# Kernel tuning notes

Hardware: AMD Instinct MI355X
Metric: run time of the kernel (lower is better)

Reference implementation:

```python
import jax, jax.numpy as jnp
import numpy as np

WS = 7           # window size
NH = 12          # num heads
EPS_ADA = 1e-6   # AdaLayerNorm eps
EPS_LN = 1e-5    # torch nn.LayerNorm default eps


def _rel_pos_index(ws):
    coords = np.stack(np.meshgrid(np.arange(ws), np.arange(ws), indexing='ij'))  # (2,ws,ws)
    flat = coords.reshape(2, -1)                      # (2, N)
    rel = flat[:, :, None] - flat[:, None, :]         # (2, N, N)
    rel = rel.transpose(1, 2, 0).astype(np.int64)     # (N, N, 2)
    rel[:, :, 0] += ws - 1
    rel[:, :, 1] += ws - 1
    rel[:, :, 0] *= 2 * ws - 1
    return jnp.asarray(rel.sum(-1))                   # (N, N) in [0, (2ws-1)^2)

REL_IDX = _rel_pos_index(WS)


def setup_inputs() -> dict:
    key = jax.random.key(0)
    ks = jax.random.split(key, 8)
    B, H, W, C, COND = 32, 56, 56, 384, 128
    L = H * W
    s = 0.02
    return {
        'x_tok': jax.random.normal(ks[0], (B, L, C), jnp.float32),
        'z_tok': jax.random.normal(ks[1], (B, L, C), jnp.float32),
        'cond': jax.random.normal(ks[2], (B, COND), jnp.float32),
        'gamma_x': jnp.ones((C,), jnp.float32),
        'beta_x': jnp.zeros((C,), jnp.float32),
        'mod_w': jax.random.normal(ks[3], (COND, 2 * C), jnp.float32) * s,
        'mod_b': jnp.zeros((2 * C,), jnp.float32),
        'gamma_z': jnp.ones((C,), jnp.float32),
        'beta_z': jnp.zeros((C,), jnp.float32),
        'rel_bias_table': jax.random.normal(ks[4], ((2 * WS - 1) ** 2, NH), jnp.float32) * s,
        'q_w': jax.random.normal(ks[5], (C, C), jnp.float32) * s,
        'q_b': jnp.zeros((C,), jnp.float32),
        'kv_w': jax.random.normal(ks[6], (C, 2 * C), jnp.float32) * s,
        'kv_b': jnp.zeros((2 * C,), jnp.float32),
        'proj_w': jax.random.normal(ks[7], (C, C), jnp.float32) * s,
        'proj_b': jnp.zeros((C,), jnp.float32),
        'H': H,
        'W': W,
    }


def reference(x_tok, z_tok, cond, gamma_x, beta_x, mod_w, mod_b,
              gamma_z, beta_z, rel_bias_table, q_w, q_b, kv_w, kv_b,
              proj_w, proj_b, H, W):
    B, L, C = x_tok.shape
    hd = C // NH
    N = WS * WS

    # AdaLayerNorm-Zero on x
    mu = x_tok.mean(-1, keepdims=True)
    var = ((x_tok - mu) ** 2).mean(-1, keepdims=True)
    x_hat = (x_tok - mu) * jax.lax.rsqrt(var + EPS_ADA)
    mod = (cond @ mod_w + mod_b).reshape(B, 2, C)
    d_gamma, d_beta = mod[:, 0], mod[:, 1]
    x = (gamma_x * (1.0 + d_gamma))[:, None, :] * x_hat + (beta_x + d_beta)[:, None, :]

    # LayerNorm on z
    mz = z_tok.mean(-1, keepdims=True)
    vz = ((z_tok - mz) ** 2).mean(-1, keepdims=True)
    z = (z_tok - mz) * jax.lax.rsqrt(vz + EPS_LN) * gamma_z + beta_z

    # window partition: (B,H,W,C) -> (B*nW, N, C)
    def part(t):
        t = t.reshape(B, H // WS, WS, W // WS, WS, C)
        return t.transpose(0, 1, 3, 2, 4, 5).reshape(-1, N, C)

    x_win = part(x.reshape(B, H, W, C))
    z_win = part(z.reshape(B, H, W, C))

    # cross window attention
    q = (x_win @ q_w + q_b).reshape(-1, N, NH, hd).transpose(0, 2, 1, 3)  # (Bw,H,N,d)
    kv = (z_win @ kv_w + kv_b).reshape(-1, N, 2, NH, hd)
    k = kv[:, :, 0].transpose(0, 2, 1, 3)
    v = kv[:, :, 1].transpose(0, 2, 1, 3)
    scale = hd ** -0.5
    attn = jnp.einsum('bhnd,bhmd->bhnm', q * scale, k)                    # (Bw,H,N,N)
    bias = rel_bias_table[REL_IDX.reshape(-1)].reshape(N, N, NH).transpose(2, 0, 1)
    attn = jax.nn.softmax(attn + bias[None], axis=-1)
    out = jnp.einsum('bhnm,bhmd->bhnd', attn, v).transpose(0, 2, 1, 3).reshape(-1, N, C)
    out = out @ proj_w + proj_b

    # window reverse: (B*nW, N, C) -> (B, L, C)
    fused = out.reshape(B, H // WS, W // WS, WS, WS, C)
    fused = fused.transpose(0, 1, 3, 2, 4, 5).reshape(B, L, C)

    return x_tok + fused
```

## Files before the change

### kernel.cpp

```cpp
#include <hip/hip_runtime.h>
#include <hip/hip_bf16.h>

typedef float f32x4 __attribute__((ext_vector_type(4)));
typedef short short8 __attribute__((ext_vector_type(8)));
typedef __hip_bfloat16 bf16;

constexpr int CDIM  = 384;
constexpr int LTOK  = 3136;
constexpr int NWIN  = 2048;
constexpr int MROWS = 100352;
constexpr int MPAD  = MROWS + 64;

__device__ __forceinline__ void gload_lds16(const void* g, void* l) {
  __builtin_amdgcn_global_load_lds(
      (const __attribute__((address_space(1))) void*)g,
      (__attribute__((address_space(3))) void*)l, 16, 0, 0);
}

__device__ __forceinline__ void row_to_bl(int r, int& b, int& l) {
  int w = r / 49, n = r % 49;
  b = w >> 6;
  int wrem = w & 63;
  int wy = wrem >> 3, wx = wrem & 7;
  int ny = n / 7, nx = n % 7;
  l = (wy * 7 + ny) * 56 + wx * 7 + nx;
}


__global__ __launch_bounds__(256) void mod_kernel(
    const float* __restrict__ cond, const float* __restrict__ mw,
    const float* __restrict__ mb, float* __restrict__ mod) {
  int idx = blockIdx.x * 256 + threadIdx.x;
  int b = idx / 768, j = idx % 768;
  float s = mb[j];
  const float* cr = cond + b * 128;
  #pragma unroll 4
  for (int k = 0; k < 128; k++) s += cr[k] * mw[(size_t)k * 768 + j];
  mod[idx] = s;
}

__global__ __launch_bounds__(256) void prep_wt(
    const float* __restrict__ qw, const float* __restrict__ kvw,
    const float* __restrict__ pw,
    bf16* __restrict__ wtq, bf16* __restrict__ wtkv, bf16* __restrict__ wtp) {
  int idx = blockIdx.x * 256 + threadIdx.x;
  const float* src; bf16* dst; int i, Wn;
  if (idx < 147456)      { i = idx;          src = qw;  dst = wtq;  Wn = 384; }
  else if (idx < 442368) { i = idx - 147456; src = kvw; dst = wtkv; Wn = 768; }
  else                   { i = idx - 442368; src = pw;  dst = wtp;  Wn = 384; }
  int chunk = i / 12288, rem = i % 12288;
  int kt = rem >> 10, rem2 = rem & 1023;
  int ni = (rem2 >> 9) & 1, g = (rem2 >> 7) & 3, r16 = (rem2 >> 3) & 15, j = rem2 & 7;
  int k = kt * 32 + g * 8 + j, n = chunk * 32 + ni * 16 + r16;
  dst[i] = __float2bfloat16(src[(size_t)k * Wn + n]);
}

__global__ __launch_bounds__(256) void bias_kernel(
    const float* __restrict__ tab, float* __restrict__ bT) {
  int idx = blockIdx.x * 256 + threadIdx.x;
  int h = idx >> 12, rem = idx & 4095, m = rem >> 6, c = rem & 63;
  float v;
  if (c >= 49)      v = -1e30f;
  else if (m >= 49) v = 0.f;
  else {
    int yq = m / 7, xq = m % 7, yk = c / 7, xk = c % 7;
    v = tab[((yq - yk + 6) * 13 + (xq - xk + 6)) * 12 + h];
  }
  bT[idx] = v;
}


struct alignas(8) B4 { bf16 h[4]; };

__global__ __launch_bounds__(256) void ln_kernel(
    const float* __restrict__ src, const float* __restrict__ gamma,
    const float* __restrict__ beta, const float* __restrict__ mod,
    float eps, bf16* __restrict__ dst) {
  int wid = threadIdx.x >> 6, lane = threadIdx.x & 63;
  int r = blockIdx.x * 4 + wid;
  int bb, ll; row_to_bl(r, bb, ll);
  const f32x4* x4 = (const f32x4*)(src + ((size_t)bb * LTOK + ll) * 384);
  f32x4 a = x4[lane];
  f32x4 b = {0.f, 0.f, 0.f, 0.f};
  if (lane < 32) b = x4[64 + lane];
  float s  = a[0] + a[1] + a[2] + a[3] + b[0] + b[1] + b[2] + b[3];
  float s2 = a[0]*a[0] + a[1]*a[1] + a[2]*a[2] + a[3]*a[3]
           + b[0]*b[0] + b[1]*b[1] + b[2]*b[2] + b[3]*b[3];
  #pragma unroll
  for (int d = 1; d < 64; d <<= 1) { s += __shfl_xor(s, d); s2 += __shfl_xor(s2, d); }
  float mu = s * (1.f / 384.f);
  float var = s2 * (1.f / 384.f) - mu * mu;
  float rstd = rsqrtf(var + eps);
  bf16* o = dst + (size_t)r * 384;
  const f32x4* g4 = (const f32x4*)gamma;
  const f32x4* be4 = (const f32x4*)beta;
  if (mod != nullptr) {
    const f32x4* mg4 = (const f32x4*)(mod + bb * 768);
    const f32x4* mb4 = (const f32x4*)(mod + bb * 768 + 384);
    {
      f32x4 gg = g4[lane], bb2 = be4[lane], mg = mg4[lane], mb = mb4[lane];
      B4 p;
      #pragma unroll
      for (int i = 0; i < 4; i++)
        p.h[i] = __float2bfloat16((gg[i] * (1.f + mg[i])) * ((a[i] - mu) * rstd) + bb2[i] + mb[i]);
      *((B4*)o + lane) = p;
    }
    if (lane < 32) {
      f32x4 gg = g4[64 + lane], bb2 = be4[64 + lane], mg = mg4[64 + lane], mb = mb4[64 + lane];
      B4 p;
      #pragma unroll
      for (int i = 0; i < 4; i++)
        p.h[i] = __float2bfloat16((gg[i] * (1.f + mg[i])) * ((b[i] - mu) * rstd) + bb2[i] + mb[i]);
      *((B4*)o + 64 + lane) = p;
    }
  } else {
    {
      f32x4 gg = g4[lane], bb2 = be4[lane];
      B4 p;
      #pragma unroll
      for (int i = 0; i < 4; i++)
        p.h[i] = __float2bfloat16((a[i] - mu) * rstd * gg[i] + bb2[i]);
      *((B4*)o + lane) = p;
    }
    if (lane < 32) {
      f32x4 gg = g4[64 + lane], bb2 = be4[64 + lane];
      B4 p;
      #pragma unroll
      for (int i = 0; i < 4; i++)
        p.h[i] = __float2bfloat16((b[i] - mu) * rstd * gg[i] + bb2[i]);
      *((B4*)o + 64 + lane) = p;
    }
  }
}


template<int MODE>
__global__ __launch_bounds__(256, 3) void gemm3(
    const bf16* __restrict__ A, const bf16* __restrict__ WTt,
    const float* __restrict__ bias, void* __restrict__ outp,
    const float* __restrict__ resid, float scale, int N) {
  __shared__ __align__(16) char Bs[2][24576];
  __shared__ float biasS[768];
  const int t = threadIdx.x;
  const int wid = t >> 6, lane = t & 63;
  const int r16 = lane & 15, g = lane >> 4;
  const int wr0 = blockIdx.x * 128 + wid * 32;

  short8 aF[2][12];
  #pragma unroll
  for (int m = 0; m < 2; m++)
    #pragma unroll
    for (int kt = 0; kt < 12; kt++)
      aF[m][kt] = *(const short8*)(A + (size_t)(wr0 + m * 16 + r16) * 384 + kt * 32 + g * 8);

  #pragma unroll
  for (int i = 0; i < 3; i++) {
    int idx = i * 256 + t;
    if (idx < N) biasS[idx] = bias[idx];
  }

  const int NCH = N >> 5;
  auto stage = [&](int c, int pb) {
    const char* srcp = (const char*)WTt + (size_t)c * 24576;
    #pragma unroll
    for (int i = 0; i < 6; i++)
      gload_lds16(srcp + i * 4096 + t * 16, Bs[pb] + i * 4096 + t * 16);
  };
  stage(0, 0);
  __syncthreads();

  constexpr int EPI = (MODE == 0) ? 16 : 32;

  for (int c = 0; c < NCH; ++c) {
    if (c + 1 < NCH) {
      stage(c + 1, (c + 1) & 1);
      asm volatile("s_waitcnt vmcnt(%0)" :: "i"(EPI + 6) : "memory");
    } else {
      asm volatile("s_waitcnt vmcnt(%0)" :: "i"(EPI) : "memory");
    }
    __builtin_amdgcn_s_barrier();
    __builtin_amdgcn_sched_barrier(0);

    const char* bufp = Bs[c & 1];
    f32x4 acc[2][2] = {};
    #pragma unroll
    for (int kt = 0; kt < 12; kt++) {
      short8 b0 = *(const short8*)(bufp + kt * 2048 + g * 256 + r16 * 16);
      short8 b1 = *(const short8*)(bufp + kt * 2048 + 1024 + g * 256 + r16 * 16);
      acc[0][0] = __builtin_amdgcn_mfma_f32_16x16x32_bf16(aF[0][kt], b0, acc[0][0], 0, 0, 0);
      acc[1][0] = __builtin_amdgcn_mfma_f32_16x16x32_bf16(aF[1][kt], b0, acc[1][0], 0, 0, 0);
      acc[0][1] = __builtin_amdgcn_mfma_f32_16x16x32_bf16(aF[0][kt], b1, acc[0][1], 0, 0, 0);
      acc[1][1] = __builtin_amdgcn_mfma_f32_16x16x32_bf16(aF[1][kt], b1, acc[1][1], 0, 0, 0);
    }
    __builtin_amdgcn_sched_barrier(0);
    __builtin_amdgcn_s_barrier();

    if (MODE == 0) {
      bf16* O = (bf16*)outp;
      #pragma unroll
      for (int ni = 0; ni < 2; ni++) {
        int col = c * 32 + ni * 16 + r16;
        float bc = biasS[col];
        #pragma unroll
        for (int m = 0; m < 2; m++) {
          int row0 = wr0 + m * 16 + g * 4;
          #pragma unroll
          for (int rr = 0; rr < 4; rr++)
            O[(size_t)(row0 + rr) * N + col] = __float2bfloat16((acc[m][ni][rr] + bc) * scale);
        }
      }
    } else {
      float* O = (float*)outp;
      #pragma unroll
      for (int m = 0; m < 2; m++) {
        #pragma unroll
        for (int rr = 0; rr < 4; rr++) {
          int row = wr0 + m * 16 + g * 4 + rr;
          int bb, ll; row_to_bl(row, bb, ll);
          size_t base = ((size_t)bb * LTOK + ll) * 384;
          #pragma unroll
          for (int ni = 0; ni < 2; ni++) {
            int col = c * 32 + ni * 16 + r16;
            O[base + col] = resid[base + col] + acc[m][ni][rr] + biasS[col];
          }
        }
      }
    }
  }
}


__global__ __launch_bounds__(64) void attn_kernel(
    const bf16* __restrict__ q, const bf16* __restrict__ kv,
    const float* __restrict__ biasT, bf16* __restrict__ o) {
  __shared__ __align__(16) bf16 vt[32][72];
  __shared__ __align__(16) bf16 P[64][72];
  const int h = blockIdx.x, w = blockIdx.y;
  const int lane = threadIdx.x;
  const int r16 = lane & 15, g = lane >> 4;
  const size_t qbase = (size_t)w * 49 * 384 + h * 32;
  const size_t kvbase = (size_t)w * 49 * 768 + h * 32;

  for (int e = lane; e < 32 * 72; e += 64) ((bf16*)vt)[e] = __float2bfloat16(0.f);
  for (int e = lane; e < 49 * 32; e += 64) {
    int c = e >> 5, d = e & 31;
    vt[d][c] = kv[kvbase + (size_t)c * 768 + 384 + d];
  }

  short8 aq[4], bk[4];
  #pragma unroll
  for (int mi = 0; mi < 4; mi++)
    aq[mi] = *(const short8*)(q + qbase + (size_t)(mi * 16 + r16) * 384 + g * 8);
  #pragma unroll
  for (int ni = 0; ni < 4; ni++)
    bk[ni] = *(const short8*)(kv + kvbase + (size_t)(ni * 16 + r16) * 768 + g * 8);

  f32x4 zero = {0.f, 0.f, 0.f, 0.f};
  f32x4 S[4][4];
  #pragma unroll
  for (int mi = 0; mi < 4; mi++)
    #pragma unroll
    for (int ni = 0; ni < 4; ni++)
      S[mi][ni] = __builtin_amdgcn_mfma_f32_16x16x32_bf16(aq[mi], bk[ni], zero, 0, 0, 0);

  const float* bt = biasT + h * 4096;
  #pragma unroll
  for (int mi = 0; mi < 4; mi++) {
    #pragma unroll
    for (int r = 0; r < 4; r++) {
      int rowm = mi * 16 + g * 4 + r;
      float sv[4];
      #pragma unroll
      for (int ni = 0; ni < 4; ni++)
        sv[ni] = S[mi][ni][r] + bt[rowm * 64 + ni * 16 + r16];
      float mx = fmaxf(fmaxf(sv[0], sv[1]), fmaxf(sv[2], sv[3]));
      #pragma unroll
      for (int d = 1; d < 16; d <<= 1) mx = fmaxf(mx, __shfl_xor(mx, d));
      float sum = 0.f;
      #pragma unroll
      for (int ni = 0; ni < 4; ni++) { sv[ni] = __expf(sv[ni] - mx); sum += sv[ni]; }
      #pragma unroll
      for (int d = 1; d < 16; d <<= 1) sum += __shfl_xor(sum, d);
      float inv = __fdividef(1.f, sum);
      #pragma unroll
      for (int ni = 0; ni < 4; ni++)
        P[rowm][ni * 16 + r16] = __float2bfloat16(sv[ni] * inv);
    }
  }
  __syncthreads();

  f32x4 acc[4][2] = {};
  #pragma unroll
  for (int c0 = 0; c0 < 2; c0++) {
    short8 ap[4], bv[2];
    #pragma unroll
    for (int mi = 0; mi < 4; mi++)
      ap[mi] = *(const short8*)((const char*)&P[0][0] + (mi * 16 + r16) * 144 + c0 * 64 + g * 16);
    #pragma unroll
    for (int di = 0; di < 2; di++)
      bv[di] = *(const short8*)((const char*)&vt[0][0] + (di * 16 + r16) * 144 + c0 * 64 + g * 16);
    #pragma unroll
    for (int mi = 0; mi < 4; mi++)
      #pragma unroll
      for (int di = 0; di < 2; di++)
        acc[mi][di] = __builtin_amdgcn_mfma_f32_16x16x32_bf16(ap[mi], bv[di], acc[mi][di], 0, 0, 0);
  }

  #pragma unroll
  for (int mi = 0; mi < 4; mi++) {
    #pragma unroll
    for (int r = 0; r < 4; r++) {
      int m = mi * 16 + g * 4 + r;
      if (m < 49) {
        #pragma unroll
        for (int di = 0; di < 2; di++)
          o[(size_t)(w * 49 + m) * 384 + h * 32 + di * 16 + r16] =
              __float2bfloat16(acc[mi][di][r]);
      }
    }
  }
}


extern "C" void kernel_launch(void* const* d_in, const int* in_sizes, int n_in,
                              void* d_out, int out_size, void* d_ws, size_t ws_size,
                              hipStream_t stream) {
  (void)in_sizes; (void)n_in; (void)out_size; (void)ws_size;
  const float* x_tok   = (const float*)d_in[0];
  const float* z_tok   = (const float*)d_in[1];
  const float* cond    = (const float*)d_in[2];
  const float* gamma_x = (const float*)d_in[3];
  const float* beta_x  = (const float*)d_in[4];
  const float* mod_w   = (const float*)d_in[5];
  const float* mod_b   = (const float*)d_in[6];
  const float* gamma_z = (const float*)d_in[7];
  const float* beta_z  = (const float*)d_in[8];
  const float* rel_tab = (const float*)d_in[9];
  const float* q_w     = (const float*)d_in[10];
  const float* q_b     = (const float*)d_in[11];
  const float* kv_w    = (const float*)d_in[12];
  const float* kv_b    = (const float*)d_in[13];
  const float* proj_w  = (const float*)d_in[14];
  const float* proj_b  = (const float*)d_in[15];

  char* ws = (char*)d_ws;
  float* modbuf = (float*)(ws + 0);
  bf16*  wtq    = (bf16*)(ws + 98304);
  bf16*  wtkv   = (bf16*)(ws + 98304 + 294912);
  bf16*  wtp    = (bf16*)(ws + 98304 + 294912 + 589824);
  float* biasT  = (float*)(ws + 98304 + 294912 + 589824 + 294912);
  char*  R1     = ws + 1474560;
  char*  R2     = R1 + (size_t)MPAD * 384 * 2;
  char*  R3     = R2 + (size_t)MPAD * 384 * 2;

  hipMemsetAsync(R2 + (size_t)MROWS * 384 * 2, 0, 64 * 384 * 2, stream);
  hipMemsetAsync(R3 + (size_t)MROWS * 768 * 2, 0, 64 * 768 * 2, stream);

  mod_kernel <<<96,   256, 0, stream>>>(cond, mod_w, mod_b, modbuf);
  prep_wt    <<<2304, 256, 0, stream>>>(q_w, kv_w, proj_w, wtq, wtkv, wtp);
  bias_kernel<<<192,  256, 0, stream>>>(rel_tab, biasT);

  ln_kernel<<<25088, 256, 0, stream>>>(x_tok, gamma_x, beta_x, modbuf, 1e-6f, (bf16*)R1);
  gemm3<0><<<784, 256, 0, stream>>>(
      (const bf16*)R1, wtq, q_b, R2, nullptr, 0.17677669529663687f, 384);
  ln_kernel<<<25088, 256, 0, stream>>>(z_tok, gamma_z, beta_z, nullptr, 1e-5f, (bf16*)R1);
  gemm3<0><<<784, 256, 0, stream>>>(
      (const bf16*)R1, wtkv, kv_b, R3, nullptr, 1.0f, 768);
  attn_kernel<<<dim3(12, NWIN), 64, 0, stream>>>(
      (const bf16*)R2, (const bf16*)R3, biasT, (bf16*)R1);
  gemm3<1><<<784, 256, 0, stream>>>(
      (const bf16*)R1, wtp, proj_b, d_out, x_tok, 1.0f, 384);
}
```

Measured before the change: 614.4 us.

## Store GEMM A operand in MFMA-tiled layout and narrow weight chunks to 16 columns

LayerNorm now writes its bf16 output directly in a tiled layout that matches the MFMA A-fragment loads, so each wave reads its A fragments with contiguous 16-byte loads instead of strided row loads. A new tile_kernel re-lays out the attention output the same way before the projection GEMM. The weight staging chunk shrinks from 32 to 16 output columns, which halves LDS per block and raises the occupancy hint from 3 to 4. The cost is an extra full pass over the attention output plus more loop iterations with less MFMA work per staged chunk.

```diff
diff --git a/kernel.cpp b/kernel.cpp
--- a/kernel.cpp
+++ b/kernel.cpp
@@ -48,10 +48,10 @@
   if (idx < 147456)      { i = idx;          src = qw;  dst = wtq;  Wn = 384; }
   else if (idx < 442368) { i = idx - 147456; src = kvw; dst = wtkv; Wn = 768; }
   else                   { i = idx - 442368; src = pw;  dst = wtp;  Wn = 384; }
-  int chunk = i / 12288, rem = i % 12288;
-  int kt = rem >> 10, rem2 = rem & 1023;
-  int ni = (rem2 >> 9) & 1, g = (rem2 >> 7) & 3, r16 = (rem2 >> 3) & 15, j = rem2 & 7;
-  int k = kt * 32 + g * 8 + j, n = chunk * 32 + ni * 16 + r16;
+  int c16 = i / 6144, rem = i % 6144;
+  int kt = rem >> 9, rem2 = rem & 511;
+  int g = rem2 >> 7, r16 = (rem2 >> 3) & 15, j = rem2 & 7;
+  int k = kt * 32 + g * 8 + j, n = c16 * 16 + r16;
   dst[i] = __float2bfloat16(src[(size_t)k * Wn + n]);
 }
 
@@ -70,88 +70,76 @@
 }
 
 
-struct alignas(8) B4 { bf16 h[4]; };
-
 __global__ __launch_bounds__(256) void ln_kernel(
     const float* __restrict__ src, const float* __restrict__ gamma,
     const float* __restrict__ beta, const float* __restrict__ mod,
-    float eps, bf16* __restrict__ dst) {
+    float eps, bf16* __restrict__ aT) {
   int wid = threadIdx.x >> 6, lane = threadIdx.x & 63;
   int r = blockIdx.x * 4 + wid;
   int bb, ll; row_to_bl(r, bb, ll);
   const f32x4* x4 = (const f32x4*)(src + ((size_t)bb * LTOK + ll) * 384);
-  f32x4 a = x4[lane];
-  f32x4 b = {0.f, 0.f, 0.f, 0.f};
-  if (lane < 32) b = x4[64 + lane];
-  float s  = a[0] + a[1] + a[2] + a[3] + b[0] + b[1] + b[2] + b[3];
-  float s2 = a[0]*a[0] + a[1]*a[1] + a[2]*a[2] + a[3]*a[3]
-           + b[0]*b[0] + b[1]*b[1] + b[2]*b[2] + b[3]*b[3];
+  const bool act = lane < 48;
+  f32x4 a = {0,0,0,0}, b = {0,0,0,0};
+  if (act) { a = x4[2 * lane]; b = x4[2 * lane + 1]; }
+  float s  = a[0]+a[1]+a[2]+a[3]+b[0]+b[1]+b[2]+b[3];
+  float s2 = a[0]*a[0]+a[1]*a[1]+a[2]*a[2]+a[3]*a[3]
+           + b[0]*b[0]+b[1]*b[1]+b[2]*b[2]+b[3]*b[3];
   #pragma unroll
   for (int d = 1; d < 64; d <<= 1) { s += __shfl_xor(s, d); s2 += __shfl_xor(s2, d); }
   float mu = s * (1.f / 384.f);
   float var = s2 * (1.f / 384.f) - mu * mu;
   float rstd = rsqrtf(var + eps);
-  bf16* o = dst + (size_t)r * 384;
-  const f32x4* g4 = (const f32x4*)gamma;
+  if (!act) return;
+  const f32x4* g4  = (const f32x4*)gamma;
   const f32x4* be4 = (const f32x4*)beta;
+  f32x4 g0 = g4[2*lane], g1 = g4[2*lane+1], b0 = be4[2*lane], b1 = be4[2*lane+1];
+  float o[8];
   if (mod != nullptr) {
     const f32x4* mg4 = (const f32x4*)(mod + bb * 768);
     const f32x4* mb4 = (const f32x4*)(mod + bb * 768 + 384);
-    {
-      f32x4 gg = g4[lane], bb2 = be4[lane], mg = mg4[lane], mb = mb4[lane];
-      B4 p;
-      #pragma unroll
-      for (int i = 0; i < 4; i++)
-        p.h[i] = __float2bfloat16((gg[i] * (1.f + mg[i])) * ((a[i] - mu) * rstd) + bb2[i] + mb[i]);
-      *((B4*)o + lane) = p;
-    }
-    if (lane < 32) {
-      f32x4 gg = g4[64 + lane], bb2 = be4[64 + lane], mg = mg4[64 + lane], mb = mb4[64 + lane];
-      B4 p;
-      #pragma unroll
-      for (int i = 0; i < 4; i++)
-        p.h[i] = __float2bfloat16((gg[i] * (1.f + mg[i])) * ((b[i] - mu) * rstd) + bb2[i] + mb[i]);
-      *((B4*)o + 64 + lane) = p;
+    f32x4 m0 = mg4[2*lane], m1 = mg4[2*lane+1], n0 = mb4[2*lane], n1 = mb4[2*lane+1];
+    #pragma unroll
+    for (int i = 0; i < 4; i++) {
+      o[i]     = (g0[i] * (1.f + m0[i])) * ((a[i] - mu) * rstd) + b0[i] + n0[i];
+      o[4 + i] = (g1[i] * (1.f + m1[i])) * ((b[i] - mu) * rstd) + b1[i] + n1[i];
     }
   } else {
-    {
-      f32x4 gg = g4[lane], bb2 = be4[lane];
-      B4 p;
-      #pragma unroll
-      for (int i = 0; i < 4; i++)
-        p.h[i] = __float2bfloat16((a[i] - mu) * rstd * gg[i] + bb2[i]);
-      *((B4*)o + lane) = p;
-    }
-    if (lane < 32) {
-      f32x4 gg = g4[64 + lane], bb2 = be4[64 + lane];
-      B4 p;
-      #pragma unroll
-      for (int i = 0; i < 4; i++)
-        p.h[i] = __float2bfloat16((b[i] - mu) * rstd * gg[i] + bb2[i]);
-      *((B4*)o + 64 + lane) = p;
-    }
-  }
+    #pragma unroll
+    for (int i = 0; i < 4; i++) {
+      o[i]     = (a[i] - mu) * rstd * g0[i] + b0[i];
+      o[4 + i] = (b[i] - mu) * rstd * g1[i] + b1[i];
+    }
+  }
+  short8 pk;
+  #pragma unroll
+  for (int i = 0; i < 8; i++)
+    pk[i] = (short)__hip_bfloat16_raw(__float2bfloat16(o[i])).x;
+  int p = r >> 7, rloc = r & 127;
+  int kt = lane >> 2, g = lane & 3;
+  *(short8*)(aT + ((size_t)(p * 12 + kt) * 4 + g) * 1024 + rloc * 8) = pk;
 }
 
 
 template<int MODE>
-__global__ __launch_bounds__(256, 3) void gemm3(
-    const bf16* __restrict__ A, const bf16* __restrict__ WTt,
+__global__ __launch_bounds__(256, 4) void gemm4(
+    const bf16* __restrict__ aT, const bf16* __restrict__ WTt,
     const float* __restrict__ bias, void* __restrict__ outp,
     const float* __restrict__ resid, float scale, int N) {
-  __shared__ __align__(16) char Bs[2][24576];
+  __shared__ __align__(16) char Bs[2][12288];
   __shared__ float biasS[768];
   const int t = threadIdx.x;
   const int wid = t >> 6, lane = t & 63;
   const int r16 = lane & 15, g = lane >> 4;
-  const int wr0 = blockIdx.x * 128 + wid * 32;
+  const int p = blockIdx.x;
+  const int wr0 = p * 128 + wid * 32;
 
   short8 aF[2][12];
   #pragma unroll
   for (int m = 0; m < 2; m++)
     #pragma unroll
     for (int kt = 0; kt < 12; kt++)
-      aF[m][kt] = *(const short8*)(A + (size_t)(wr0 + m * 16 + r16) * 384 + kt * 32 + g * 8);
+      aF[m][kt] = *(const short8*)(aT + ((size_t)(p * 12 + kt) * 4 + g) * 1024
+                                       + (wid * 32 + m * 16 + r16) * 8);
 
   #pragma unroll
   for (int i = 0; i < 3; i++) {
@@ -159,22 +147,22 @@
     if (idx < N) biasS[idx] = bias[idx];
   }
 
-  const int NCH = N >> 5;
+  const int NCH = N >> 4;
   auto stage = [&](int c, int pb) {
-    const char* srcp = (const char*)WTt + (size_t)c * 24576;
-    #pragma unroll
-    for (int i = 0; i < 6; i++)
-      gload_lds16(srcp + i * 4096 + t * 16, Bs[pb] + i * 4096 + t * 16);
+    const char* srcp = (const char*)WTt + (size_t)c * 12288;
+    #pragma unroll
+    for (int i = 0; i < 3; i++)
+      gload_lds16(srcp + (i * 256 + t) * 16, Bs[pb] + (i * 256 + t) * 16);
   };
   stage(0, 0);
   __syncthreads();
 
-  constexpr int EPI = (MODE == 0) ? 16 : 32;
+  constexpr int EPI = (MODE == 0) ? 8 : 16;
 
   for (int c = 0; c < NCH; ++c) {
     if (c + 1 < NCH) {
       stage(c + 1, (c + 1) & 1);
-      asm volatile("s_waitcnt vmcnt(%0)" :: "i"(EPI + 6) : "memory");
+      asm volatile("s_waitcnt vmcnt(%0)" :: "i"(EPI + 3) : "memory");
     } else {
       asm volatile("s_waitcnt vmcnt(%0)" :: "i"(EPI) : "memory");
     }
@@ -182,35 +170,31 @@
     __builtin_amdgcn_sched_barrier(0);
 
     const char* bufp = Bs[c & 1];
-    f32x4 acc[2][2] = {};
+    f32x4 acc[2] = {};
     #pragma unroll
     for (int kt = 0; kt < 12; kt++) {
-      short8 b0 = *(const short8*)(bufp + kt * 2048 + g * 256 + r16 * 16);
-      short8 b1 = *(const short8*)(bufp + kt * 2048 + 1024 + g * 256 + r16 * 16);
-      acc[0][0] = __builtin_amdgcn_mfma_f32_16x16x32_bf16(aF[0][kt], b0, acc[0][0], 0, 0, 0);
-      acc[1][0] = __builtin_amdgcn_mfma_f32_16x16x32_bf16(aF[1][kt], b0, acc[1][0], 0, 0, 0);
-      acc[0][1] = __builtin_amdgcn_mfma_f32_16x16x32_bf16(aF[0][kt], b1, acc[0][1], 0, 0, 0);
-      acc[1][1] = __builtin_amdgcn_mfma_f32_16x16x32_bf16(aF[1][kt], b1, acc[1][1], 0, 0, 0);
+      short8 bF = *(const short8*)(bufp + kt * 1024 + g * 256 + r16 * 16);
+      acc[0] = __builtin_amdgcn_mfma_f32_16x16x32_bf16(aF[0][kt], bF, acc[0], 0, 0, 0);
+      acc[1] = __builtin_amdgcn_mfma_f32_16x16x32_bf16(aF[1][kt], bF, acc[1], 0, 0, 0);
     }
     __builtin_amdgcn_sched_barrier(0);
     __builtin_amdgcn_s_barrier();
 
     if (MODE == 0) {
       bf16* O = (bf16*)outp;
-      #pragma unroll
-      for (int ni = 0; ni < 2; ni++) {
-        int col = c * 32 + ni * 16 + r16;
-        float bc = biasS[col];
+      int col = c * 16 + r16;
+      float bc = biasS[col];
+      #pragma unroll
+      for (int m = 0; m < 2; m++) {
+        int row0 = wr0 + m * 16 + g * 4;
         #pragma unroll
-        for (int m = 0; m < 2; m++) {
-          int row0 = wr0 + m * 16 + g * 4;
-          #pragma unroll
-          for (int rr = 0; rr < 4; rr++)
-            O[(size_t)(row0 + rr) * N + col] = __float2bfloat16((acc[m][ni][rr] + bc) * scale);
-        }
+        for (int rr = 0; rr < 4; rr++)
+          O[(size_t)(row0 + rr) * N + col] = __float2bfloat16((acc[m][rr] + bc) * scale);
       }
     } else {
       float* O = (float*)outp;
+      int col = c * 16 + r16;
+      float bc = biasS[col];
       #pragma unroll
       for (int m = 0; m < 2; m++) {
         #pragma unroll
@@ -218,11 +202,7 @@
           int row = wr0 + m * 16 + g * 4 + rr;
           int bb, ll; row_to_bl(row, bb, ll);
           size_t base = ((size_t)bb * LTOK + ll) * 384;
-          #pragma unroll
-          for (int ni = 0; ni < 2; ni++) {
-            int col = c * 32 + ni * 16 + r16;
-            O[base + col] = resid[base + col] + acc[m][ni][rr] + biasS[col];
-          }
+          O[base + col] = resid[base + col] + acc[m][rr] + bc;
         }
       }
     }
@@ -319,6 +299,17 @@
       }
     }
   }
+}
+
+__global__ __launch_bounds__(256) void tile_kernel(
+    const bf16* __restrict__ src, bf16* __restrict__ aT) {
+  int wid = threadIdx.x >> 6, lane = threadIdx.x & 63;
+  int r = blockIdx.x * 4 + wid;
+  if (lane >= 48) return;
+  short8 v = *(const short8*)(src + (size_t)r * 384 + lane * 8);
+  int p = r >> 7, rloc = r & 127;
+  int kt = lane >> 2, g = lane & 3;
+  *(short8*)(aT + ((size_t)(p * 12 + kt) * 4 + g) * 1024 + rloc * 8) = v;
 }
 
 
@@ -352,6 +343,7 @@
   char*  R1     = ws + 1474560;
   char*  R2     = R1 + (size_t)MPAD * 384 * 2;
   char*  R3     = R2 + (size_t)MPAD * 384 * 2;
+  char*  R4     = R3 + (size_t)MPAD * 768 * 2;
 
   hipMemsetAsync(R2 + (size_t)MROWS * 384 * 2, 0, 64 * 384 * 2, stream);
   hipMemsetAsync(R3 + (size_t)MROWS * 768 * 2, 0, 64 * 768 * 2, stream);
@@ -361,13 +353,14 @@
   bias_kernel<<<192,  256, 0, stream>>>(rel_tab, biasT);
 
   ln_kernel<<<25088, 256, 0, stream>>>(x_tok, gamma_x, beta_x, modbuf, 1e-6f, (bf16*)R1);
-  gemm3<0><<<784, 256, 0, stream>>>(
+  gemm4<0><<<784, 256, 0, stream>>>(
       (const bf16*)R1, wtq, q_b, R2, nullptr, 0.17677669529663687f, 384);
   ln_kernel<<<25088, 256, 0, stream>>>(z_tok, gamma_z, beta_z, nullptr, 1e-5f, (bf16*)R1);
-  gemm3<0><<<784, 256, 0, stream>>>(
+  gemm4<0><<<784, 256, 0, stream>>>(
       (const bf16*)R1, wtkv, kv_b, R3, nullptr, 1.0f, 768);
   attn_kernel<<<dim3(12, NWIN), 64, 0, stream>>>(
       (const bf16*)R2, (const bf16*)R3, biasT, (bf16*)R1);
-  gemm3<1><<<784, 256, 0, stream>>>(
-      (const bf16*)R1, wtp, proj_b, d_out, x_tok, 1.0f, 384);
-}
+  tile_kernel<<<25088, 256, 0, stream>>>((const bf16*)R1, (bf16*)R4);
+  gemm4<1><<<784, 256, 0, stream>>>(
+      (const bf16*)R4, wtp, proj_b, d_out, x_tok, 1.0f, 384);
+}
```

New measurement: 807.8 us. 31.5% more time.
